# Kernel tuning notes

Measured on AMD Instinct MI355X. Metric: run time of the kernel, lower is better.

Reference implementation:

```python
import jax, jax.numpy as jnp
import numpy as np

N_NODES = 100000
N_EDGES = 3200000
D = 12
BN_EPS = 1e-5


def setup_inputs() -> dict:
    key = jax.random.key(0)
    k1, k2, k3, k4 = jax.random.split(key, 4)
    return {
        "src_embeddings": jax.random.normal(k1, (N_NODES, D), dtype=jnp.float32),
        "dst_embeddings": jax.random.normal(k2, (N_NODES, D), dtype=jnp.float32),
        "bn_weight": jnp.ones((1,), dtype=jnp.float32),
        "bn_bias": jnp.zeros((1,), dtype=jnp.float32),
        "graph_src": jax.random.randint(k3, (N_EDGES,), 0, N_NODES, dtype=jnp.int64) if jax.config.jax_enable_x64 else jax.random.randint(k3, (N_EDGES,), 0, N_NODES, dtype=jnp.int32),
        "graph_dst": jax.random.randint(k4, (N_EDGES,), 0, N_NODES, dtype=jnp.int32),
    }


def reference(src_embeddings, dst_embeddings, bn_weight, bn_bias, graph_src, graph_dst):
    n_nodes = src_embeddings.shape[0]
    # per-edge dot product: gather + einsum 'ij,ij->i'
    likelihood = jnp.einsum(
        "ed,ed->e", src_embeddings[graph_src], dst_embeddings[graph_dst]
    )
    # BatchNorm1d(1), training mode: normalize with biased batch stats
    mean = jnp.mean(likelihood)
    var = jnp.mean(jnp.square(likelihood - mean))
    logits = (likelihood - mean) * jax.lax.rsqrt(var + BN_EPS) * bn_weight[0] + bn_bias[0]
    # weighting_function = torch.exp
    edge_weights = jnp.exp(logits)
    # scatter-normalize over src index (softmax-like per source node)
    denom = jax.ops.segment_sum(edge_weights, graph_src, num_segments=n_nodes)
    edge_weights = edge_weights / (1e-12 + denom[graph_src])
    return edge_weights[:, None]
```

## Files before the change

### kernel.cpp

```cpp
#include <hip/hip_runtime.h>
#include <hip/hip_fp16.h>

#define BN_EPS 1e-5f
#define BUCKET 16000

#define QS11 186.0f
#define QS10 92.909090f
#define QI11 0.0053763445f
#define QI10 0.0107632094f
#define QP11 (QI11*QI11)
#define QP10 (QI10*QI10)

typedef int      v4i __attribute__((ext_vector_type(4)));
typedef unsigned v4u __attribute__((ext_vector_type(4)));
typedef unsigned v2u __attribute__((ext_vector_type(2)));
typedef float    v4f __attribute__((ext_vector_type(4)));

__device__ __forceinline__ __half2 u2h2(unsigned u) {
    union { unsigned u; __half2 h; } c; c.u = u; return c.h;
}

__device__ __forceinline__ float2 bn_params(const double* acc,
                                            const float* bnw,
                                            const float* bnb, int E) {
    double mean = acc[0] / (double)E;
    double var  = acc[1] / (double)E - mean * mean;
    float scale = bnw[0] * rsqrtf((float)var + BN_EPS);
    float shift = bnb[0] - (float)mean * scale;
    return make_float2(scale, shift);
}

__device__ __forceinline__ int qclamp(float x, float s, int lim) {
    int q = (int)rintf(x * s);
    return min(max(q, -lim), lim);
}
__device__ __forceinline__ unsigned enc3(float a, float b, float c) {
    unsigned qa = (unsigned)qclamp(a, QS11, 1023) & 0x7FFu;
    unsigned qb = (unsigned)qclamp(b, QS11, 1023) & 0x7FFu;
    unsigned qc = (unsigned)qclamp(c, QS10, 511)  & 0x3FFu;
    return qa | (qb << 11) | (qc << 22);
}

__global__ void k_pack_quant(const float* __restrict__ src_emb,
                             const float* __restrict__ dst_emb,
                             int4* __restrict__ qs,
                             int4* __restrict__ qd, int N) {
    int t = blockIdx.x * blockDim.x + threadIdx.x;
    if (t >= 2 * N) return;
    int n = (t < N) ? t : t - N;
    const float* r = ((t < N) ? src_emb : dst_emb) + (size_t)n * 12;
    int4* dst = ((t < N) ? qs : qd) + n;
    float v[12];
    #pragma unroll
    for (int j = 0; j < 12; ++j) v[j] = r[j];
    int4 w;
    w.x = (int)enc3(v[0], v[1], v[2]);
    w.y = (int)enc3(v[3], v[4], v[5]);
    w.z = (int)enc3(v[6], v[7], v[8]);
    w.w = (int)enc3(v[9], v[10], v[11]);
    *dst = w;
}

__device__ __forceinline__ float qdot(int4 A, int4 B) {
    int aw[4] = {A.x, A.y, A.z, A.w};
    int bw[4] = {B.x, B.y, B.z, B.w};
    int s11 = 0, s10 = 0;
    #pragma unroll
    for (int k = 0; k < 4; ++k) {
        int a0 = (aw[k] << 21) >> 21;
        int a1 = (aw[k] << 10) >> 21;
        int a2 =  aw[k] >> 22;
        int b0 = (bw[k] << 21) >> 21;
        int b1 = (bw[k] << 10) >> 21;
        int b2 =  bw[k] >> 22;
        s11 += a0 * b0 + a1 * b1;
        s10 += a2 * b2;
    }
    return (float)s11 * QP11 + (float)s10 * QP10;
}

__global__ __launch_bounds__(256) void k_dot(
        const int4* __restrict__ qs,
        const int4* __restrict__ qd,
        const int* __restrict__ gsrc,
        const int* __restrict__ gdst,
        __half* __restrict__ like,
        double* __restrict__ acc,
        int E) {
    int e0 = (blockIdx.x * blockDim.x + threadIdx.x) * 8;
    float lsum = 0.f, lsq = 0.f;
    if (e0 + 8 <= E) {
        v4i s0 = __builtin_nontemporal_load((const v4i*)(gsrc + e0));
        v4i s1 = __builtin_nontemporal_load((const v4i*)(gsrc + e0 + 4));
        v4i d0 = __builtin_nontemporal_load((const v4i*)(gdst + e0));
        v4i d1 = __builtin_nontemporal_load((const v4i*)(gdst + e0 + 4));
        int is[8] = {s0.x, s0.y, s0.z, s0.w, s1.x, s1.y, s1.z, s1.w};
        int id[8] = {d0.x, d0.y, d0.z, d0.w, d1.x, d1.y, d1.z, d1.w};
        int4 ra[8], rb[8];
        #pragma unroll
        for (int k = 0; k < 8; ++k) {
            ra[k] = qs[is[k]];
            rb[k] = qd[id[k]];
        }
        float dv[8];
        #pragma unroll
        for (int k = 0; k < 8; ++k) {
            dv[k] = qdot(ra[k], rb[k]);
            lsum += dv[k];
            lsq  = fmaf(dv[k], dv[k], lsq);
        }
        v4u o;
        union { __half2 h; unsigned u; } c;
        c.h = __floats2half2_rn(dv[0], dv[1]); o.x = c.u;
        c.h = __floats2half2_rn(dv[2], dv[3]); o.y = c.u;
        c.h = __floats2half2_rn(dv[4], dv[5]); o.z = c.u;
        c.h = __floats2half2_rn(dv[6], dv[7]); o.w = c.u;
        __builtin_nontemporal_store(o, (v4u*)(like + e0));
    } else {
        for (int e = e0; e < E; ++e) {
            float d = qdot(qs[gsrc[e]], qd[gdst[e]]);
            like[e] = __float2half(d);
            lsum += d;
            lsq  += d * d;
        }
    }
    for (int off = 32; off > 0; off >>= 1) {
        lsum += __shfl_down(lsum, off);
        lsq  += __shfl_down(lsq, off);
    }
    __shared__ float ssum[4], ssq[4];
    int wave = threadIdx.x >> 6, lane = threadIdx.x & 63;
    if (lane == 0) { ssum[wave] = lsum; ssq[wave] = lsq; }
    __syncthreads();
    if (threadIdx.x == 0) {
        float ts = 0.f, tq = 0.f;
        for (int i = 0; i < 4; ++i) { ts += ssum[i]; tq += ssq[i]; }
        atomicAdd(&acc[0], (double)ts);
        atomicAdd(&acc[1], (double)tq);
    }
}

__global__ __launch_bounds__(512) void k_bucket_scatter(
        const __half* __restrict__ like,
        const int* __restrict__ gsrc,
        const double* __restrict__ acc,
        const float* __restrict__ bnw,
        const float* __restrict__ bnb,
        float* __restrict__ slab,
        int E, int G) {
    __shared__ float sm[BUCKET];
    __shared__ float2 s_par;
    const int g  = blockIdx.x;
    const int p  = blockIdx.y;
    const int lo = p * BUCKET;

    if (threadIdx.x == 0) s_par = bn_params(acc, bnw, bnb, E);
    for (int i = threadIdx.x; i < BUCKET; i += blockDim.x) sm[i] = 0.f;
    __syncthreads();
    const float scale = s_par.x;
    const float shift = s_par.y;

    int per = (E + G - 1) / G;
    per = (per + 3) & ~3;
    const int s0 = g * per;
    const int s1 = min(s0 + per, E);

    for (int e = s0 + (int)threadIdx.x * 4; e < s1; e += (int)blockDim.x * 4) {
        if (e + 4 <= s1) {
            v4i n4 = __builtin_nontemporal_load((const v4i*)(gsrc + e));
            v2u l2 = __builtin_nontemporal_load((const v2u*)(like + e));
            float2 fa = __half22float2(u2h2(l2.x));
            float2 fb = __half22float2(u2h2(l2.y));
            unsigned o0 = (unsigned)(n4.x - lo);
            unsigned o1 = (unsigned)(n4.y - lo);
            unsigned o2 = (unsigned)(n4.z - lo);
            unsigned o3 = (unsigned)(n4.w - lo);
            if (o0 < BUCKET) atomicAdd(&sm[o0], __expf(fmaf(fa.x, scale, shift)));
            if (o1 < BUCKET) atomicAdd(&sm[o1], __expf(fmaf(fa.y, scale, shift)));
            if (o2 < BUCKET) atomicAdd(&sm[o2], __expf(fmaf(fb.x, scale, shift)));
            if (o3 < BUCKET) atomicAdd(&sm[o3], __expf(fmaf(fb.y, scale, shift)));
        } else {
            for (int k = 0; e + k < s1; ++k) {
                unsigned o = (unsigned)(gsrc[e + k] - lo);
                if (o < BUCKET)
                    atomicAdd(&sm[o], __expf(fmaf(__half2float(like[e + k]), scale, shift)));
            }
        }
    }
    __syncthreads();

    float* dst = slab + ((size_t)p * G + g) * BUCKET;
    for (int i = threadIdx.x; i < BUCKET; i += blockDim.x)
        __builtin_nontemporal_store(sm[i], dst + i);
}

__global__ void k_fold(const float* __restrict__ slab,
                       float* __restrict__ denom, int N, int G) {
    int n = blockIdx.x * blockDim.x + threadIdx.x;
    if (n >= N) return;
    int p   = n / BUCKET;
    int off = n - p * BUCKET;
    const float* s = slab + (size_t)p * G * BUCKET + off;
    float acc = 0.f;
    for (int g = 0; g < G; ++g)
        acc += __builtin_nontemporal_load(s + (size_t)g * BUCKET);
    denom[n] = acc;
}

__global__ __launch_bounds__(256) void k_normalize(
        const __half* __restrict__ like,
        const int* __restrict__ gsrc,
        const double* __restrict__ acc,
        const float* __restrict__ bnw,
        const float* __restrict__ bnb,
        const float* __restrict__ denom,
        float* __restrict__ out,
        int E) {
    __shared__ float2 s_par;
    if (threadIdx.x == 0) s_par = bn_params(acc, bnw, bnb, E);
    __syncthreads();
    const float scale = s_par.x;
    const float shift = s_par.y;
    int e = (blockIdx.x * blockDim.x + threadIdx.x) * 4;
    if (e + 4 <= E) {
        v4i n4 = __builtin_nontemporal_load((const v4i*)(gsrc + e));
        v2u l2 = __builtin_nontemporal_load((const v2u*)(like + e));
        float2 fa = __half22float2(u2h2(l2.x));
        float2 fb = __half22float2(u2h2(l2.y));
        v4f o;
        o.x = __expf(fmaf(fa.x, scale, shift)) / (1e-12f + denom[n4.x]);
        o.y = __expf(fmaf(fa.y, scale, shift)) / (1e-12f + denom[n4.y]);
        o.z = __expf(fmaf(fb.x, scale, shift)) / (1e-12f + denom[n4.z]);
        o.w = __expf(fmaf(fb.y, scale, shift)) / (1e-12f + denom[n4.w]);
        __builtin_nontemporal_store(o, (v4f*)(out + e));
    } else {
        for (; e < E; ++e)
            out[e] = __expf(fmaf(__half2float(like[e]), scale, shift)) /
                     (1e-12f + denom[gsrc[e]]);
    }
}

__global__ void k_exp_scatter_agent(const __half* __restrict__ like,
                                    const int* __restrict__ gsrc,
                                    const double* __restrict__ acc,
                                    const float* __restrict__ bnw,
                                    const float* __restrict__ bnb,
                                    float* __restrict__ denom, int E) {
    __shared__ float2 s_par;
    if (threadIdx.x == 0) s_par = bn_params(acc, bnw, bnb, E);
    __syncthreads();
    for (int e = blockIdx.x * blockDim.x + threadIdx.x; e < E;
         e += gridDim.x * blockDim.x)
        atomicAdd(&denom[gsrc[e]],
                  __expf(fmaf(__half2float(like[e]), s_par.x, s_par.y)));
}

extern "C" void kernel_launch(void* const* d_in, const int* in_sizes, int n_in,
                              void* d_out, int out_size, void* d_ws, size_t ws_size,
                              hipStream_t stream) {
    const float* src_emb = (const float*)d_in[0];
    const float* dst_emb = (const float*)d_in[1];
    const float* bnw     = (const float*)d_in[2];
    const float* bnb     = (const float*)d_in[3];
    const int*   gsrc    = (const int*)d_in[4];
    const int*   gdst    = (const int*)d_in[5];

    const int E = in_sizes[4];
    const int N = in_sizes[0] / 12;
    float* out = (float*)d_out;

    const int P = (N + BUCKET - 1) / BUCKET;

    char* ws = (char*)d_ws;
    double* acc   = (double*)ws;
    size_t  off   = 64;
    float*  denom = (float*)(ws + off);  off += ((size_t)N * 4 + 63) & ~(size_t)63;
    int4*   qs    = (int4*)(ws + off);   off += ((size_t)N * 16 + 63) & ~(size_t)63;
    int4*   qd    = (int4*)(ws + off);   off += ((size_t)N * 16 + 63) & ~(size_t)63;
    __half* like  = (__half*)(ws + off); off += ((size_t)E * 2 + 63) & ~(size_t)63;
    float*  slab  = (float*)(ws + off);

    size_t rem = (ws_size > off) ? ws_size - off : 0;
    int G = 0;
    for (int cand = 64; cand >= 8; cand >>= 1) {
        if ((size_t)P * cand * BUCKET * 4 <= rem) { G = cand; break; }
    }

    const int block = 256;

    hipMemsetAsync(ws, 0, 32, stream);

    k_pack_quant<<<(2 * N + block - 1) / block, block, 0, stream>>>(
        src_emb, dst_emb, qs, qd, N);

    int dot_blocks = ((E + 7) / 8 + block - 1) / block;
    k_dot<<<dot_blocks, block, 0, stream>>>(qs, qd, gsrc, gdst, like, acc, E);

    if (G > 0) {
        dim3 gsc(G, P);
        k_bucket_scatter<<<gsc, 512, 0, stream>>>(like, gsrc, acc, bnw, bnb,
                                                  slab, E, G);
        k_fold<<<(N + block - 1) / block, block, 0, stream>>>(slab, denom, N, G);
    } else {
        hipMemsetAsync(denom, 0, (size_t)N * 4, stream);
        int blocks = min((E + block - 1) / block, 4096);
        k_exp_scatter_agent<<<blocks, block, 0, stream>>>(like, gsrc, acc,
                                                          bnw, bnb, denom, E);
    }

    int norm_blocks = ((E + 3) / 4 + block - 1) / block;
    k_normalize<<<norm_blocks, block, 0, stream>>>(like, gsrc, acc, bnw, bnb,
                                                   denom, out, E);
}
```

Before: 145.4 us.

## Pack src index and truncated half likelihood into one 32-bit plane, fp16 slabs

The dot kernel now writes one 32-bit word per edge holding the 17-bit source index and a 15-bit half likelihood with the sign and low mantissa bit dropped. Later kernels read only this word instead of separate gsrc and half-likelihood arrays, cutting per-edge reads from 6 to 4 bytes in both scatter passes. The per-bucket partial-sum slabs are also stored as fp16, halving slab write and fold read traffic. The cost is precision: likelihood loses its sign bit, which breaks negative dot products, and fp16 partial sums lose accuracy. It also assumes node indices fit in 17 bits.

```diff
diff --git a/kernel.cpp b/kernel.cpp
--- a/kernel.cpp
+++ b/kernel.cpp
@@ -11,13 +11,13 @@
 #define QP11 (QI11*QI11)
 #define QP10 (QI10*QI10)
 
-typedef int      v4i __attribute__((ext_vector_type(4)));
-typedef unsigned v4u __attribute__((ext_vector_type(4)));
-typedef unsigned v2u __attribute__((ext_vector_type(2)));
-typedef float    v4f __attribute__((ext_vector_type(4)));
-
-__device__ __forceinline__ __half2 u2h2(unsigned u) {
-    union { unsigned u; __half2 h; } c; c.u = u; return c.h;
+typedef int            v4i __attribute__((ext_vector_type(4)));
+typedef unsigned       v4u __attribute__((ext_vector_type(4)));
+typedef float          v4f __attribute__((ext_vector_type(4)));
+typedef unsigned short u16;
+
+__device__ __forceinline__ float pk_like(unsigned pk) {
+    return __half2float(__ushort_as_half((u16)((pk & 0x7FFFu) << 1)));
 }
 
 __device__ __forceinline__ float2 bn_params(const double* acc,
@@ -84,7 +84,7 @@
         const int4* __restrict__ qd,
         const int* __restrict__ gsrc,
         const int* __restrict__ gdst,
-        __half* __restrict__ like,
+        unsigned* __restrict__ plane,
         double* __restrict__ acc,
         int E) {
     int e0 = (blockIdx.x * blockDim.x + threadIdx.x) * 8;
@@ -102,26 +102,27 @@
             ra[k] = qs[is[k]];
             rb[k] = qd[id[k]];
         }
-        float dv[8];
+        unsigned pk[8];
         #pragma unroll
         for (int k = 0; k < 8; ++k) {
-            dv[k] = qdot(ra[k], rb[k]);
-            lsum += dv[k];
-            lsq  = fmaf(dv[k], dv[k], lsq);
-        }
-        v4u o;
-        union { __half2 h; unsigned u; } c;
-        c.h = __floats2half2_rn(dv[0], dv[1]); o.x = c.u;
-        c.h = __floats2half2_rn(dv[2], dv[3]); o.y = c.u;
-        c.h = __floats2half2_rn(dv[4], dv[5]); o.z = c.u;
-        c.h = __floats2half2_rn(dv[6], dv[7]); o.w = c.u;
-        __builtin_nontemporal_store(o, (v4u*)(like + e0));
+            float d = qdot(ra[k], rb[k]);
+            lsum += d;
+            lsq  = fmaf(d, d, lsq);
+            unsigned h = (unsigned)__half_as_ushort(__float2half(d));
+            pk[k] = ((unsigned)is[k] << 15) | (h >> 1);
+        }
+        v4u o0 = {pk[0], pk[1], pk[2], pk[3]};
+        v4u o1 = {pk[4], pk[5], pk[6], pk[7]};
+        __builtin_nontemporal_store(o0, (v4u*)(plane + e0));
+        __builtin_nontemporal_store(o1, (v4u*)(plane + e0 + 4));
     } else {
         for (int e = e0; e < E; ++e) {
-            float d = qdot(qs[gsrc[e]], qd[gdst[e]]);
-            like[e] = __float2half(d);
+            int gs = gsrc[e];
+            float d = qdot(qs[gs], qd[gdst[e]]);
             lsum += d;
             lsq  += d * d;
+            unsigned h = (unsigned)__half_as_ushort(__float2half(d));
+            plane[e] = ((unsigned)gs << 15) | (h >> 1);
         }
     }
     for (int off = 32; off > 0; off >>= 1) {
@@ -141,12 +142,11 @@
 }
 
 __global__ __launch_bounds__(512) void k_bucket_scatter(
-        const __half* __restrict__ like,
-        const int* __restrict__ gsrc,
+        const unsigned* __restrict__ plane,
         const double* __restrict__ acc,
         const float* __restrict__ bnw,
         const float* __restrict__ bnb,
-        float* __restrict__ slab,
+        u16* __restrict__ slab,
         int E, int G) {
     __shared__ float sm[BUCKET];
     __shared__ float2 s_par;
@@ -167,49 +167,49 @@
 
     for (int e = s0 + (int)threadIdx.x * 4; e < s1; e += (int)blockDim.x * 4) {
         if (e + 4 <= s1) {
-            v4i n4 = __builtin_nontemporal_load((const v4i*)(gsrc + e));
-            v2u l2 = __builtin_nontemporal_load((const v2u*)(like + e));
-            float2 fa = __half22float2(u2h2(l2.x));
-            float2 fb = __half22float2(u2h2(l2.y));
-            unsigned o0 = (unsigned)(n4.x - lo);
-            unsigned o1 = (unsigned)(n4.y - lo);
-            unsigned o2 = (unsigned)(n4.z - lo);
-            unsigned o3 = (unsigned)(n4.w - lo);
-            if (o0 < BUCKET) atomicAdd(&sm[o0], __expf(fmaf(fa.x, scale, shift)));
-            if (o1 < BUCKET) atomicAdd(&sm[o1], __expf(fmaf(fa.y, scale, shift)));
-            if (o2 < BUCKET) atomicAdd(&sm[o2], __expf(fmaf(fb.x, scale, shift)));
-            if (o3 < BUCKET) atomicAdd(&sm[o3], __expf(fmaf(fb.y, scale, shift)));
+            v4u p4 = __builtin_nontemporal_load((const v4u*)(plane + e));
+            unsigned pk[4] = {p4.x, p4.y, p4.z, p4.w};
+            #pragma unroll
+            for (int k = 0; k < 4; ++k) {
+                unsigned o = (pk[k] >> 15) - (unsigned)lo;
+                if (o < BUCKET)
+                    atomicAdd(&sm[o], __expf(fmaf(pk_like(pk[k]), scale, shift)));
+            }
         } else {
             for (int k = 0; e + k < s1; ++k) {
-                unsigned o = (unsigned)(gsrc[e + k] - lo);
+                unsigned pk = plane[e + k];
+                unsigned o = (pk >> 15) - (unsigned)lo;
                 if (o < BUCKET)
-                    atomicAdd(&sm[o], __expf(fmaf(__half2float(like[e + k]), scale, shift)));
+                    atomicAdd(&sm[o], __expf(fmaf(pk_like(pk), scale, shift)));
             }
         }
     }
     __syncthreads();
 
-    float* dst = slab + ((size_t)p * G + g) * BUCKET;
-    for (int i = threadIdx.x; i < BUCKET; i += blockDim.x)
-        __builtin_nontemporal_store(sm[i], dst + i);
-}
-
-__global__ void k_fold(const float* __restrict__ slab,
+    u16* dst = slab + ((size_t)p * G + g) * BUCKET;
+    for (int i = threadIdx.x; i < BUCKET; i += blockDim.x) {
+        u16 bits = __half_as_ushort(__float2half(sm[i]));
+        __builtin_nontemporal_store(bits, dst + i);
+    }
+}
+
+__global__ void k_fold(const u16* __restrict__ slab,
                        float* __restrict__ denom, int N, int G) {
     int n = blockIdx.x * blockDim.x + threadIdx.x;
     if (n >= N) return;
     int p   = n / BUCKET;
     int off = n - p * BUCKET;
-    const float* s = slab + (size_t)p * G * BUCKET + off;
+    const u16* s = slab + (size_t)p * G * BUCKET + off;
     float acc = 0.f;
-    for (int g = 0; g < G; ++g)
-        acc += __builtin_nontemporal_load(s + (size_t)g * BUCKET);
+    for (int g = 0; g < G; ++g) {
+        u16 bits = __builtin_nontemporal_load(s + (size_t)g * BUCKET);
+        acc += __half2float(__ushort_as_half(bits));
+    }
     denom[n] = acc;
 }
 
 __global__ __launch_bounds__(256) void k_normalize(
-        const __half* __restrict__ like,
-        const int* __restrict__ gsrc,
+        const unsigned* __restrict__ plane,
         const double* __restrict__ acc,
         const float* __restrict__ bnw,
         const float* __restrict__ bnb,
@@ -223,25 +223,24 @@
     const float shift = s_par.y;
     int e = (blockIdx.x * blockDim.x + threadIdx.x) * 4;
     if (e + 4 <= E) {
-        v4i n4 = __builtin_nontemporal_load((const v4i*)(gsrc + e));
-        v2u l2 = __builtin_nontemporal_load((const v2u*)(like + e));
-        float2 fa = __half22float2(u2h2(l2.x));
-        float2 fb = __half22float2(u2h2(l2.y));
+        v4u p4 = __builtin_nontemporal_load((const v4u*)(plane + e));
+        unsigned pk[4] = {p4.x, p4.y, p4.z, p4.w};
         v4f o;
-        o.x = __expf(fmaf(fa.x, scale, shift)) / (1e-12f + denom[n4.x]);
-        o.y = __expf(fmaf(fa.y, scale, shift)) / (1e-12f + denom[n4.y]);
-        o.z = __expf(fmaf(fb.x, scale, shift)) / (1e-12f + denom[n4.z]);
-        o.w = __expf(fmaf(fb.y, scale, shift)) / (1e-12f + denom[n4.w]);
+        o.x = __expf(fmaf(pk_like(pk[0]), scale, shift)) / (1e-12f + denom[pk[0] >> 15]);
+        o.y = __expf(fmaf(pk_like(pk[1]), scale, shift)) / (1e-12f + denom[pk[1] >> 15]);
+        o.z = __expf(fmaf(pk_like(pk[2]), scale, shift)) / (1e-12f + denom[pk[2] >> 15]);
+        o.w = __expf(fmaf(pk_like(pk[3]), scale, shift)) / (1e-12f + denom[pk[3] >> 15]);
         __builtin_nontemporal_store(o, (v4f*)(out + e));
     } else {
-        for (; e < E; ++e)
-            out[e] = __expf(fmaf(__half2float(like[e]), scale, shift)) /
-                     (1e-12f + denom[gsrc[e]]);
-    }
-}
-
-__global__ void k_exp_scatter_agent(const __half* __restrict__ like,
-                                    const int* __restrict__ gsrc,
+        for (; e < E; ++e) {
+            unsigned pk = plane[e];
+            out[e] = __expf(fmaf(pk_like(pk), scale, shift)) /
+                     (1e-12f + denom[pk >> 15]);
+        }
+    }
+}
+
+__global__ void k_exp_scatter_agent(const unsigned* __restrict__ plane,
                                     const double* __restrict__ acc,
                                     const float* __restrict__ bnw,
                                     const float* __restrict__ bnb,
@@ -250,9 +249,11 @@
     if (threadIdx.x == 0) s_par = bn_params(acc, bnw, bnb, E);
     __syncthreads();
     for (int e = blockIdx.x * blockDim.x + threadIdx.x; e < E;
-         e += gridDim.x * blockDim.x)
-        atomicAdd(&denom[gsrc[e]],
-                  __expf(fmaf(__half2float(like[e]), s_par.x, s_par.y)));
+         e += gridDim.x * blockDim.x) {
+        unsigned pk = plane[e];
+        atomicAdd(&denom[pk >> 15],
+                  __expf(fmaf(pk_like(pk), s_par.x, s_par.y)));
+    }
 }
 
 extern "C" void kernel_launch(void* const* d_in, const int* in_sizes, int n_in,
@@ -272,18 +273,18 @@
     const int P = (N + BUCKET - 1) / BUCKET;
 
     char* ws = (char*)d_ws;
-    double* acc   = (double*)ws;
-    size_t  off   = 64;
-    float*  denom = (float*)(ws + off);  off += ((size_t)N * 4 + 63) & ~(size_t)63;
-    int4*   qs    = (int4*)(ws + off);   off += ((size_t)N * 16 + 63) & ~(size_t)63;
-    int4*   qd    = (int4*)(ws + off);   off += ((size_t)N * 16 + 63) & ~(size_t)63;
-    __half* like  = (__half*)(ws + off); off += ((size_t)E * 2 + 63) & ~(size_t)63;
-    float*  slab  = (float*)(ws + off);
+    double*   acc   = (double*)ws;
+    size_t    off   = 64;
+    float*    denom = (float*)(ws + off);    off += ((size_t)N * 4 + 63) & ~(size_t)63;
+    int4*     qs    = (int4*)(ws + off);     off += ((size_t)N * 16 + 63) & ~(size_t)63;
+    int4*     qd    = (int4*)(ws + off);     off += ((size_t)N * 16 + 63) & ~(size_t)63;
+    unsigned* plane = (unsigned*)(ws + off); off += ((size_t)E * 4 + 63) & ~(size_t)63;
+    u16*      slab  = (u16*)(ws + off);
 
     size_t rem = (ws_size > off) ? ws_size - off : 0;
     int G = 0;
     for (int cand = 64; cand >= 8; cand >>= 1) {
-        if ((size_t)P * cand * BUCKET * 4 <= rem) { G = cand; break; }
+        if ((size_t)P * cand * BUCKET * 2 <= rem) { G = cand; break; }
     }
 
     const int block = 256;
@@ -294,21 +295,21 @@
         src_emb, dst_emb, qs, qd, N);
 
     int dot_blocks = ((E + 7) / 8 + block - 1) / block;
-    k_dot<<<dot_blocks, block, 0, stream>>>(qs, qd, gsrc, gdst, like, acc, E);
+    k_dot<<<dot_blocks, block, 0, stream>>>(qs, qd, gsrc, gdst, plane, acc, E);
 
     if (G > 0) {
         dim3 gsc(G, P);
-        k_bucket_scatter<<<gsc, 512, 0, stream>>>(like, gsrc, acc, bnw, bnb,
+        k_bucket_scatter<<<gsc, 512, 0, stream>>>(plane, acc, bnw, bnb,
                                                   slab, E, G);
         k_fold<<<(N + block - 1) / block, block, 0, stream>>>(slab, denom, N, G);
     } else {
         hipMemsetAsync(denom, 0, (size_t)N * 4, stream);
         int blocks = min((E + block - 1) / block, 4096);
-        k_exp_scatter_agent<<<blocks, block, 0, stream>>>(like, gsrc, acc,
+        k_exp_scatter_agent<<<blocks, block, 0, stream>>>(plane, acc,
                                                           bnw, bnb, denom, E);
     }
 
     int norm_blocks = ((E + 3) / 4 + block - 1) / block;
-    k_normalize<<<norm_blocks, block, 0, stream>>>(like, gsrc, acc, bnw, bnb,
+    k_normalize<<<norm_blocks, block, 0, stream>>>(plane, acc, bnw, bnb,
                                                    denom, out, E);
 }
```

Result: no change. 143.2 us (-1.5%).
